# Kernel tuning notes

Measured on AMD Instinct MI355X. Metric: run time of the kernel, lower is better.

Reference implementation:

```python
import jax, jax.numpy as jnp
import numpy as np

N_NODES = 100000
N_EDGES = 1600000
IN_DIM, HID_DIM, LAT_DIM = 128, 64, 32


def glorot(key, fan_in, fan_out):
    lim = np.sqrt(6.0 / (fan_in + fan_out)).astype(np.float32)
    return jax.random.uniform(key, (fan_in, fan_out), jnp.float32, -lim, lim)


def setup_inputs() -> dict:
    key = jax.random.key(0)
    ks = jax.random.split(key, 10)
    x = jax.random.normal(ks[0], (N_NODES, IN_DIM), jnp.float32)
    edge_index = jax.random.randint(ks[1], (2, N_EDGES), 0, N_NODES, jnp.int64)
    return {
        "x": x,
        "edge_index": edge_index,
        "W1": glorot(ks[2], IN_DIM, HID_DIM), "b1": jnp.zeros((HID_DIM,), jnp.float32),
        "W2": glorot(ks[3], HID_DIM, LAT_DIM), "b2": jnp.zeros((LAT_DIM,), jnp.float32),
        "W3": glorot(ks[4], LAT_DIM, HID_DIM), "b3": jnp.zeros((HID_DIM,), jnp.float32),
        "W4": glorot(ks[5], HID_DIM, IN_DIM), "b4": jnp.zeros((IN_DIM,), jnp.float32),
    }


def gcn_conv(x, W, b, src, dst, norm_edge, norm_self):
    # x' = D^{-1/2} (A + I) D^{-1/2} x W + b  (PyG GCNConv, add_self_loops=True)
    h = x @ W                                   # [N, out]
    msg = h[src] * norm_edge[:, None]           # [E, out] gather + scale
    agg = jax.ops.segment_sum(msg, dst, num_segments=x.shape[0])  # scatter-add
    agg = agg + h * norm_self[:, None]          # self-loop contribution
    return agg + b


def reference(x, edge_index, W1, b1, W2, b2, W3, b3, W4, b4):
    src, dst = edge_index[0], edge_index[1]
    n = x.shape[0]
    # degree includes self-loop (+1); symmetric normalization
    deg = jax.ops.segment_sum(jnp.ones_like(dst, dtype=x.dtype), dst, num_segments=n) + 1.0
    dinv = jax.lax.rsqrt(deg)
    norm_edge = dinv[src] * dinv[dst]           # [E]
    norm_self = dinv * dinv                     # [N]

    # encode (dropout is identity in eval mode)
    h = jax.nn.relu(gcn_conv(x, W1, b1, src, dst, norm_edge, norm_self))
    z = gcn_conv(h, W2, b2, src, dst, norm_edge, norm_self)
    # decode
    h = jax.nn.relu(gcn_conv(z, W3, b3, src, dst, norm_edge, norm_self))
    x_rec = gcn_conv(h, W4, b4, src, dst, norm_edge, norm_self)
    return (x_rec, z)
```

## Files before the change

kernel.cpp:

```cpp
#include <hip/hip_runtime.h>
#include <hip/hip_bf16.h>

constexpr int N_NODES = 100000;
constexpr int N_EDGES = 1600000;
constexpr int SCAN_B  = 1024;
constexpr int SCAN_G  = (N_NODES + SCAN_B) / SCAN_B;
constexpr int FCH     = 8192;
constexpr int NCH     = (N_EDGES + FCH - 1) / FCH;
constexpr int SLICE_N = N_NODES / 8;
constexpr int PADC    = 48;

constexpr size_t OFF_FLAG = 0;
constexpr size_t OFF_DEG  = 4    * 1024;
constexpr size_t OFF_DINV = 408  * 1024;
constexpr size_t OFF_OFFS = 812  * 1024;
constexpr size_t OFF_CURS = 1216 * 1024;
constexpr size_t OFF_BSUM = 1620 * 1024;
constexpr size_t OFF_WC   = 1624 * 1024;
constexpr size_t OFF_CSR  = 1712 * 1024;
constexpr size_t OFF_A    = 8192 * 1024;
constexpr size_t OFF_B    = 21504ul * 1024;

constexpr size_t OFF_PAD  = 1792ul  * 1024;
constexpr size_t OFF_A2   = 20544ul * 1024;
constexpr size_t OFF_B2   = 33044ul * 1024;
constexpr size_t NEED_PAD = OFF_B2 + (size_t)N_NODES * 64 * 2;
static_assert(OFF_PAD >= OFF_WC + 20768 * 4, "pad must not clobber Wc");
static_assert(OFF_A2 >= OFF_PAD + (size_t)N_NODES * PADC * 4, "A2 overlaps pad");
static_assert(OFF_B2 >= OFF_A2 + (size_t)N_NODES * 64 * 2, "B2 overlaps A2");

constexpr int BUK_SH  = 9;
constexpr int BUK_N   = 512;
constexpr int NBUK    = (N_NODES + BUK_N - 1) / BUK_N;
constexpr int BUKCAP  = 10240;
constexpr int P1_CH   = 4096;
constexpr int P1_BLK  = (N_EDGES + P1_CH - 1) / P1_CH;
static_assert((size_t)NBUK * BUKCAP * 8 <= (size_t)N_NODES * 64 * 2 * 2, "ebuf fits A2+B2");
static_assert(NBUK * 4 <= 4096, "bucket cursors fit BSUM region");
static_assert((BUK_N * PADC * 4) % 64 == 0, "pad rows line-aligned per bucket");

constexpr int WC_W1 = 0, WC_W2 = 8192, WC_W3 = 10240, WC_W4 = 12288;
constexpr int WC_B1 = 20480, WC_B2 = 20544, WC_B3 = 20576, WC_B4 = 20640;
constexpr int WC_TOT = 20768;

__device__ __forceinline__ float bf2f(unsigned short b) {
    union { unsigned u; float f; } c; c.u = ((unsigned)b) << 16; return c.f;
}

__device__ __forceinline__ short f2bf(float f) {
    union { float f; unsigned u; } c; c.f = f;
    return (short)((c.u + 0x7FFFu + ((c.u >> 16) & 1u)) >> 16);
}

__device__ __forceinline__ int ntload(const int* p) {
    return __builtin_nontemporal_load(p);
}

__global__ void detect_kernel(const unsigned* __restrict__ w1raw,
                              const unsigned* __restrict__ eiraw,
                              int* __restrict__ flags) {
    const int t = threadIdx.x;
    int f32 = 0, i32 = 0;
    for (int i = t; i < 1024; i += 256) {
        unsigned lo = w1raw[i] & 0xFFFFu;
        if ((lo & 0x7F80u) >= 0x3F00u) f32 = 1;
    }
    for (int i = t; i < 4096; i += 256)
        if ((i & 1) && eiraw[i] != 0u) i32 = 1;
    if (f32) atomicOr(&flags[0], 1);
    if (i32) atomicOr(&flags[1], 1);
}

__device__ __forceinline__ unsigned edge_src(const int* ei, int i64, int e) {
    return (unsigned)(i64 ? ntload(&ei[2 * (size_t)e]) : ntload(&ei[e]));
}
__device__ __forceinline__ unsigned edge_dst(const int* ei, int i64, int e) {
    return (unsigned)(i64 ? ntload(&ei[2 * (size_t)N_EDGES + 2 * (size_t)e])
                          : ntload(&ei[(size_t)N_EDGES + e]));
}

__global__ void convw_kernel(const void* W1, const void* b1, const void* W2, const void* b2,
                             const void* W3, const void* b3, const void* W4, const void* b4,
                             const int* __restrict__ flags, float* __restrict__ Wc) {
    int i = blockIdx.x * blockDim.x + threadIdx.x;
    if (i >= WC_TOT) return;
    const void* src; int off;
    if      (i < WC_W2) { src = W1; off = i; }
    else if (i < WC_W3) { src = W2; off = i - WC_W2; }
    else if (i < WC_W4) { src = W3; off = i - WC_W3; }
    else if (i < WC_B1) { src = W4; off = i - WC_W4; }
    else if (i < WC_B2) { src = b1; off = i - WC_B1; }
    else if (i < WC_B3) { src = b2; off = i - WC_B2; }
    else if (i < WC_B4) { src = b3; off = i - WC_B3; }
    else                { src = b4; off = i - WC_B4; }
    Wc[i] = flags[0] ? ((const float*)src)[off]
                     : __bfloat162float(((const __hip_bfloat16*)src)[off]);
}

__global__ __launch_bounds__(256) void bsort1_kernel(
        const int* __restrict__ ei, const int* __restrict__ flags,
        int* __restrict__ gcur, int2* __restrict__ ebuf) {
    __shared__ int hist[NBUK], base[NBUK], cur[NBUK];
    const int i64 = (flags[1] == 0);
    for (int i = threadIdx.x; i < NBUK; i += 256) { hist[i] = 0; cur[i] = 0; }
    __syncthreads();
    const int e0 = blockIdx.x * P1_CH;
    const int e1 = min(e0 + P1_CH, N_EDGES);
    for (int e = e0 + threadIdx.x; e < e1; e += 256) {
        const unsigned d = edge_dst(ei, i64, e);
        const unsigned s = edge_src(ei, i64, e);
        if (d < (unsigned)N_NODES && s < (unsigned)N_NODES)
            atomicAdd(&hist[d >> BUK_SH], 1);
    }
    __syncthreads();
    for (int b = threadIdx.x; b < NBUK; b += 256)
        base[b] = hist[b] ? atomicAdd(&gcur[b], hist[b]) : 0;
    __syncthreads();
    for (int e = e0 + threadIdx.x; e < e1; e += 256) {
        const unsigned d = edge_dst(ei, i64, e);
        const unsigned s = edge_src(ei, i64, e);
        if (d < (unsigned)N_NODES && s < (unsigned)N_NODES) {
            const int b = (int)(d >> BUK_SH);
            const int p = base[b] + atomicAdd(&cur[b], 1);
            if (p < BUKCAP) ebuf[(size_t)b * BUKCAP + p] = make_int2((int)s, (int)d);
        }
    }
}

__global__ __launch_bounds__(1024) void bsort2_kernel(
        const int* __restrict__ gcur, const int2* __restrict__ ebuf,
        int* __restrict__ cnt, int* __restrict__ pad, float* __restrict__ dinv) {
    __shared__ int lc[BUK_N];
    const int b  = blockIdx.x;
    const int n0 = b * BUK_N;
    const int nn = min(BUK_N, N_NODES - n0);
    if (threadIdx.x < BUK_N) lc[threadIdx.x] = 0;
    __syncthreads();
    const int ne = min(gcur[b], BUKCAP);
    for (int i = threadIdx.x; i < ne; i += 1024) {
        const int2 p = ebuf[(size_t)b * BUKCAP + i];
        const int pos = atomicAdd(&lc[p.y - n0], 1);
        if (pos < PADC) pad[(size_t)p.y * PADC + pos] = p.x;
    }
    __syncthreads();
    for (int t = threadIdx.x; t < nn; t += 1024) {
        const int c = lc[t];
        cnt[n0 + t]  = c;
        dinv[n0 + t] = rsqrtf((float)c + 1.0f);
    }
}

__global__ void deg_kernel(const int* __restrict__ ei, const int* __restrict__ flags,
                           int* __restrict__ deg) {
    const int slice = blockIdx.x & 7;
    const int chunk = blockIdx.x >> 3;
    const int i64 = (flags[1] == 0);
    const unsigned lo = (unsigned)(slice * SLICE_N);
    const int e0 = chunk * FCH;
    const int e1 = min(e0 + FCH, N_EDGES);
    for (int e = e0 + threadIdx.x; e < e1; e += 256) {
        unsigned d = edge_dst(ei, i64, e);
        if (d - lo < (unsigned)SLICE_N && d < (unsigned)N_NODES) atomicAdd(&deg[d], 1);
    }
}

__global__ void dinv_kernel(const int* __restrict__ deg, float* __restrict__ dinv) {
    int n = blockIdx.x * blockDim.x + threadIdx.x;
    if (n < N_NODES) dinv[n] = rsqrtf((float)deg[n] + 1.0f);
}

__global__ __launch_bounds__(1024) void scan1_kernel(const int* __restrict__ deg,
                                                     int* __restrict__ bsum) {
    const int i = blockIdx.x * SCAN_B + threadIdx.x;
    const int lane = threadIdx.x & 63, wid = threadIdx.x >> 6;
    int v = (i < N_NODES) ? deg[i] : 0;
    for (int o = 32; o > 0; o >>= 1) v += __shfl_down(v, o, 64);
    __shared__ int ws[16];
    if (lane == 0) ws[wid] = v;
    __syncthreads();
    if (wid == 0) {
        int t = (lane < 16) ? ws[lane] : 0;
        for (int o = 8; o > 0; o >>= 1) t += __shfl_down(t, o, 64);
        if (lane == 0) bsum[blockIdx.x] = t;
    }
}

__global__ void scan2_kernel(const int* __restrict__ bsum, int* __restrict__ boff) {
    const int t = threadIdx.x;
    __shared__ int tmp[128];
    int v = (t < SCAN_G) ? bsum[t] : 0;
    tmp[t] = v;
    __syncthreads();
    for (int o = 1; o < 128; o <<= 1) {
        int a = (t >= o) ? tmp[t - o] : 0;
        __syncthreads();
        tmp[t] += a;
        __syncthreads();
    }
    boff[t] = tmp[t] - v;
}

__global__ __launch_bounds__(1024) void scan3_kernel(const int* __restrict__ deg,
                                                     const int* __restrict__ boff,
                                                     int* __restrict__ offs,
                                                     int* __restrict__ curs) {
    const int i = blockIdx.x * SCAN_B + threadIdx.x;
    const int lane = threadIdx.x & 63, wid = threadIdx.x >> 6;
    int v = (i < N_NODES) ? deg[i] : 0;
    int incl = v;
    for (int o = 1; o < 64; o <<= 1) {
        int t = __shfl_up(incl, (unsigned)o, 64);
        if (lane >= o) incl += t;
    }
    __shared__ int wsum[16], woff[16];
    if (lane == 63) wsum[wid] = incl;
    __syncthreads();
    if (wid == 0 && lane < 16) {
        int u = wsum[lane];
        int uin = u;
        for (int o = 1; o < 16; o <<= 1) {
            int t = __shfl_up(uin, (unsigned)o, 64);
            if (lane >= o) uin += t;
        }
        woff[lane] = uin - u;
    }
    __syncthreads();
    const int excl = incl - v + woff[wid] + boff[blockIdx.x];
    if (i <= N_NODES) {
        offs[i] = excl;
        if (i < N_NODES) curs[i] = excl;
    }
}

__global__ void fill_kernel(const int* __restrict__ ei, const int* __restrict__ flags,
                            int* __restrict__ curs, int* __restrict__ csr) {
    const int slice = blockIdx.x & 7;
    const int chunk = blockIdx.x >> 3;
    const int i64 = (flags[1] == 0);
    const unsigned lo = (unsigned)(slice * SLICE_N);
    const int e0 = chunk * FCH;
    const int e1 = min(e0 + FCH, N_EDGES);
    for (int e = e0 + threadIdx.x; e < e1; e += 256) {
        unsigned d = edge_dst(ei, i64, e);
        if (d - lo < (unsigned)SLICE_N && d < (unsigned)N_NODES) {
            unsigned s = edge_src(ei, i64, e);
            if (s < (unsigned)N_NODES) {
                int pos = atomicAdd(&curs[d], 1);
                if ((unsigned)pos < (unsigned)N_EDGES) csr[pos] = (int)s;
            }
        }
    }
}

typedef __attribute__((ext_vector_type(8))) short bf16x8;
typedef __attribute__((ext_vector_type(4))) float f32x4;

constexpr int NTILES    = N_NODES / 16;
constexpr int GEMM_GRID = 512;
static_assert(N_NODES % 16 == 0, "tile grid requires multiple of 16");

template <int IN, int OUT, bool DYNIN, bool RELU, bool BIAS, bool SCALE, bool HASWS, bool HASG>
__global__ __launch_bounds__(256) void gemm_mfma(
        const void* __restrict__ in, int inLD, const int* __restrict__ flags,
        const float* __restrict__ Wc, int WLD, const float* __restrict__ bias,
        const float* __restrict__ dinv,
        __hip_bfloat16* __restrict__ wsout,
        void* __restrict__ gout, int gLD) {
    constexpr int KS = IN / 32;
    constexpr int NT = OUT / 16;
    static_assert(IN % 32 == 0 && OUT % 16 == 0, "shape");
    const int lane = threadIdx.x & 63;
    const int wid  = threadIdx.x >> 6;
    const int m = lane & 15;
    const int g = lane >> 4;
    const int f32f = flags[0];

    bf16x8 bfrag[NT][KS];
#pragma unroll
    for (int t = 0; t < NT; ++t) {
#pragma unroll
        for (int ks = 0; ks < KS; ++ks) {
            const float* wp = Wc + (size_t)(ks * 32 + g * 8) * WLD + t * 16 + m;
            bf16x8 b;
#pragma unroll
            for (int j = 0; j < 8; ++j) b[j] = f2bf(wp[(size_t)j * WLD]);
            bfrag[t][ks] = b;
        }
    }
    float bb[NT];
    if (BIAS) {
#pragma unroll
        for (int t = 0; t < NT; ++t) bb[t] = bias[t * 16 + m];
    }

    for (int tile = blockIdx.x * 4 + wid; tile < NTILES; tile += GEMM_GRID * 4) {
        f32x4 acc[NT];
#pragma unroll
        for (int t = 0; t < NT; ++t) {
            const float b0 = BIAS ? bb[t] : 0.0f;
            acc[t] = (f32x4){b0, b0, b0, b0};
        }
        const size_t arow = (size_t)tile * 16 + m;
#pragma unroll
        for (int ks = 0; ks < KS; ++ks) {
            bf16x8 af;
            if (DYNIN && f32f) {
                const float* xp = (const float*)in + arow * inLD + ks * 32 + g * 8;
                const float4 v0 = *(const float4*)xp;
                const float4 v1 = *(const float4*)(xp + 4);
                af[0] = f2bf(v0.x); af[1] = f2bf(v0.y);
                af[2] = f2bf(v0.z); af[3] = f2bf(v0.w);
                af[4] = f2bf(v1.x); af[5] = f2bf(v1.y);
                af[6] = f2bf(v1.z); af[7] = f2bf(v1.w);
            } else {
                af = *(const bf16x8*)((const __hip_bfloat16*)in + arow * inLD + ks * 32 + g * 8);
            }
#pragma unroll
            for (int t = 0; t < NT; ++t)
                acc[t] = __builtin_amdgcn_mfma_f32_16x16x32_bf16(af, bfrag[t][ks], acc[t], 0, 0, 0);
        }
        const int rbase = tile * 16 + g * 4;
        float di[4];
        if (SCALE) {
#pragma unroll
            for (int r = 0; r < 4; ++r) di[r] = dinv[rbase + r];
        }
#pragma unroll
        for (int t = 0; t < NT; ++t) {
            const int col = t * 16 + m;
#pragma unroll
            for (int r = 0; r < 4; ++r) {
                float v = acc[t][r];
                if (RELU) v = fmaxf(v, 0.0f);
                if (SCALE) v *= di[r];
                const size_t row = (size_t)(rbase + r);
                if (HASWS) wsout[row * OUT + col] = __float2bfloat16(v);
                if (HASG) {
                    const size_t gi = row * gLD + col;
                    if (f32f) ((float*)gout)[gi] = v;
                    else      ((__hip_bfloat16*)gout)[gi] = __float2bfloat16(v);
                }
            }
        }
    }
}

template <int D, int SUBW, bool RELU, bool PADDED>
__global__ __launch_bounds__(256) void agg_kernel(
        const int* __restrict__ base, const int* __restrict__ adj,
        const float* __restrict__ dinv,
        const __hip_bfloat16* __restrict__ h,
        const float* __restrict__ bias,
        __hip_bfloat16* __restrict__ wsout,
        __hip_bfloat16* __restrict__ wsout_sc,
        void* __restrict__ gout, size_t gbase, int gLD,
        const int* __restrict__ flags) {
    const int lane = threadIdx.x & 63;
    const int wid  = threadIdx.x >> 6;
    constexpr int SPW = 64 / SUBW;
    constexpr int SPB = 4 * SPW;
    const int n = blockIdx.x * SPB + wid * SPW + (SUBW == 64 ? 0 : (lane >> 5));
    if (n >= N_NODES) return;
    const int sl = lane & (SUBW - 1);
    const int col = sl;
    float acc = __bfloat162float(h[(size_t)n * D + col]);
    int o0, o1;
    if (PADDED) {
        o0 = n * PADC;
        o1 = o0 + min(base[n], PADC);
    } else {
        o0 = base[n]; o1 = base[n + 1];
    }
    for (int bse = o0; bse < o1; bse += SUBW) {
        const int idx = bse + sl;
        const int sid = (idx < o1) ? adj[idx] : 0;
        const int cnt = min(SUBW, o1 - bse);
        int k = 0;
        for (; k + 8 <= cnt; k += 8) {
            int s[8];
#pragma unroll
            for (int u = 0; u < 8; ++u) s[u] = __shfl(sid, k + u, SUBW);
            float v[8];
#pragma unroll
            for (int u = 0; u < 8; ++u) v[u] = __bfloat162float(h[(size_t)s[u] * D + col]);
            acc += ((v[0] + v[1]) + (v[2] + v[3])) + ((v[4] + v[5]) + (v[6] + v[7]));
        }
        for (; k < cnt; ++k) {
            const int s = __shfl(sid, k, SUBW);
            acc += __bfloat162float(h[(size_t)s * D + col]);
        }
    }
    const float di = dinv[n];
    float v = acc * di;
    if (bias) v += bias[col];
    if (RELU) v = fmaxf(v, 0.0f);
    if (wsout)    wsout[(size_t)n * D + col]    = __float2bfloat16(v);
    if (wsout_sc) wsout_sc[(size_t)n * D + col] = __float2bfloat16(v * di);
    if (gout) {
        const size_t gi = gbase + (size_t)n * gLD + col;
        if (flags[0]) ((float*)gout)[gi] = v;
        else          ((__hip_bfloat16*)gout)[gi] = __float2bfloat16(v);
    }
}

template <bool P>
static inline void run_layers(const void* x, const int* flags, float* Wc, float* dinv,
                              const int* base, const int* adj,
                              __hip_bfloat16* A, __hip_bfloat16* B,
                              void* d_out, hipStream_t stream) {
    gemm_mfma<128, 64, true, false, false, true, true, false><<<GEMM_GRID, 256, 0, stream>>>(
        x, 128, flags, Wc + WC_W1, 64, nullptr, dinv, A, nullptr, 0);
    agg_kernel<64, 64, true, P><<<(N_NODES + 3) / 4, 256, 0, stream>>>(
        base, adj, dinv, A, Wc + WC_B1, B, nullptr, nullptr, 0, 0, flags);

    gemm_mfma<64, 32, false, false, false, true, true, false><<<GEMM_GRID, 256, 0, stream>>>(
        B, 64, flags, Wc + WC_W2, 32, nullptr, dinv, A, nullptr, 0);
    agg_kernel<32, 32, false, P><<<(N_NODES + 7) / 8, 256, 0, stream>>>(
        base, adj, dinv, A, Wc + WC_B2, nullptr, B,
        d_out, (size_t)N_NODES * 128, 32, flags);

    agg_kernel<32, 32, false, P><<<(N_NODES + 7) / 8, 256, 0, stream>>>(
        base, adj, dinv, B, nullptr, A, nullptr, nullptr, 0, 0, flags);
    gemm_mfma<32, 64, false, true, true, true, true, false><<<GEMM_GRID, 256, 0, stream>>>(
        A, 32, flags, Wc + WC_W3, 64, Wc + WC_B3, dinv, B, nullptr, 0);

    agg_kernel<64, 64, false, P><<<(N_NODES + 3) / 4, 256, 0, stream>>>(
        base, adj, dinv, B, nullptr, A, nullptr, nullptr, 0, 0, flags);
    gemm_mfma<64, 128, false, false, true, false, false, true><<<GEMM_GRID, 256, 0, stream>>>(
        A, 64, flags, Wc + WC_W4, 128, Wc + WC_B4, dinv, nullptr, d_out, 128);
}

extern "C" void kernel_launch(void* const* d_in, const int* in_sizes, int n_in,
                              void* d_out, int out_size, void* d_ws, size_t ws_size,
                              hipStream_t stream) {
    const void* x  = d_in[0];
    const int* ei  = (const int*)d_in[1];
    const void* W1 = d_in[2]; const void* b1 = d_in[3];
    const void* W2 = d_in[4]; const void* b2 = d_in[5];
    const void* W3 = d_in[6]; const void* b3 = d_in[7];
    const void* W4 = d_in[8]; const void* b4 = d_in[9];

    char* ws = (char*)d_ws;
    int*   flags = (int*)(ws + OFF_FLAG);
    int*   cnt   = (int*)(ws + OFF_DEG);
    float* dinv  = (float*)(ws + OFF_DINV);
    float* Wc    = (float*)(ws + OFF_WC);

    hipMemsetAsync(flags, 0, 2 * sizeof(int), stream);
    hipMemsetAsync(cnt, 0, (size_t)N_NODES * sizeof(int), stream);
    detect_kernel<<<1, 256, 0, stream>>>((const unsigned*)W1, (const unsigned*)ei, flags);
    convw_kernel<<<(WC_TOT + 255) / 256, 256, 0, stream>>>(W1, b1, W2, b2, W3, b3, W4, b4,
                                                           flags, Wc);

    if (ws_size >= NEED_PAD) {
        int*  pad  = (int*)(ws + OFF_PAD);
        int*  gcur = (int*)(ws + OFF_BSUM);
        int2* ebuf = (int2*)(ws + OFF_A2);
        __hip_bfloat16* A = (__hip_bfloat16*)(ws + OFF_A2);
        __hip_bfloat16* B = (__hip_bfloat16*)(ws + OFF_B2);
        hipMemsetAsync(gcur, 0, NBUK * sizeof(int), stream);
        bsort1_kernel<<<P1_BLK, 256, 0, stream>>>(ei, flags, gcur, ebuf);
        bsort2_kernel<<<NBUK, 1024, 0, stream>>>(gcur, ebuf, cnt, pad, dinv);
        run_layers<true>(x, flags, Wc, dinv, cnt, pad, A, B, d_out, stream);
    } else {
        int*   offs  = (int*)(ws + OFF_OFFS);
        int*   curs  = (int*)(ws + OFF_CURS);
        int*   bsum  = (int*)(ws + OFF_BSUM);
        int*   boff  = bsum + 128;
        int*   csr   = (int*)(ws + OFF_CSR);
        __hip_bfloat16* A = (__hip_bfloat16*)(ws + OFF_A);
        __hip_bfloat16* B = (__hip_bfloat16*)(ws + OFF_B);
        deg_kernel<<<8 * NCH, 256, 0, stream>>>(ei, flags, cnt);
        dinv_kernel<<<(N_NODES + 255) / 256, 256, 0, stream>>>(cnt, dinv);
        scan1_kernel<<<SCAN_G, SCAN_B, 0, stream>>>(cnt, bsum);
        scan2_kernel<<<1, 128, 0, stream>>>(bsum, boff);
        scan3_kernel<<<SCAN_G, SCAN_B, 0, stream>>>(cnt, boff, offs, curs);
        fill_kernel<<<8 * NCH, 256, 0, stream>>>(ei, flags, curs, csr);
        run_layers<false>(x, flags, Wc, dinv, offs, csr, A, B, d_out, stream);
    }
}
```

Measured before the change: 392.6 us.

## Fuse aggregation with small GEMMs and pack bucket-sort edge records

```diff
diff --git a/kernel.cpp b/kernel.cpp
--- a/kernel.cpp
+++ b/kernel.cpp
@@ -35,9 +35,9 @@
 constexpr int BUKCAP  = 10240;
 constexpr int P1_CH   = 4096;
 constexpr int P1_BLK  = (N_EDGES + P1_CH - 1) / P1_CH;
-static_assert((size_t)NBUK * BUKCAP * 8 <= (size_t)N_NODES * 64 * 2 * 2, "ebuf fits A2+B2");
+static_assert((size_t)NBUK * BUKCAP * 4 <= (size_t)N_NODES * 64 * 2, "ebuf fits A2");
 static_assert(NBUK * 4 <= 4096, "bucket cursors fit BSUM region");
-static_assert((BUK_N * PADC * 4) % 64 == 0, "pad rows line-aligned per bucket");
+static_assert(NBUK < 255, "bucket id fits uchar with 0xFF sentinel");
 
 constexpr int WC_W1 = 0, WC_W2 = 8192, WC_W3 = 10240, WC_W4 = 12288;
 constexpr int WC_B1 = 20480, WC_B2 = 20544, WC_B3 = 20576, WC_B4 = 20640;
@@ -99,36 +99,42 @@
 
 __global__ __launch_bounds__(256) void bsort1_kernel(
         const int* __restrict__ ei, const int* __restrict__ flags,
-        int* __restrict__ gcur, int2* __restrict__ ebuf) {
-    __shared__ int hist[NBUK], base[NBUK], cur[NBUK];
+        int* __restrict__ gcur, int* __restrict__ ebuf) {
+    __shared__ int hist[NBUK], rbase[NBUK], cur[NBUK];
+    __shared__ int pk[P1_CH];
+    __shared__ unsigned char bk[P1_CH];
     const int i64 = (flags[1] == 0);
     for (int i = threadIdx.x; i < NBUK; i += 256) { hist[i] = 0; cur[i] = 0; }
     __syncthreads();
     const int e0 = blockIdx.x * P1_CH;
-    const int e1 = min(e0 + P1_CH, N_EDGES);
-    for (int e = e0 + threadIdx.x; e < e1; e += 256) {
-        const unsigned d = edge_dst(ei, i64, e);
-        const unsigned s = edge_src(ei, i64, e);
-        if (d < (unsigned)N_NODES && s < (unsigned)N_NODES)
-            atomicAdd(&hist[d >> BUK_SH], 1);
-    }
-    __syncthreads();
-    for (int b = threadIdx.x; b < NBUK; b += 256)
-        base[b] = hist[b] ? atomicAdd(&gcur[b], hist[b]) : 0;
-    __syncthreads();
-    for (int e = e0 + threadIdx.x; e < e1; e += 256) {
-        const unsigned d = edge_dst(ei, i64, e);
-        const unsigned s = edge_src(ei, i64, e);
+    const int ne = min(P1_CH, N_EDGES - e0);
+    for (int i = threadIdx.x; i < ne; i += 256) {
+        const unsigned d = edge_dst(ei, i64, e0 + i);
+        const unsigned s = edge_src(ei, i64, e0 + i);
         if (d < (unsigned)N_NODES && s < (unsigned)N_NODES) {
             const int b = (int)(d >> BUK_SH);
-            const int p = base[b] + atomicAdd(&cur[b], 1);
-            if (p < BUKCAP) ebuf[(size_t)b * BUKCAP + p] = make_int2((int)s, (int)d);
+            atomicAdd(&hist[b], 1);
+            bk[i] = (unsigned char)b;
+            pk[i] = (int)(((d & (BUK_N - 1)) << 17) | s);
+        } else {
+            bk[i] = 0xFF;
+        }
+    }
+    __syncthreads();
+    for (int b = threadIdx.x; b < NBUK; b += 256)
+        rbase[b] = hist[b] ? atomicAdd(&gcur[b], hist[b]) : 0;
+    __syncthreads();
+    for (int i = threadIdx.x; i < ne; i += 256) {
+        const int b = bk[i];
+        if (b != 0xFF) {
+            const int p = rbase[b] + atomicAdd(&cur[b], 1);
+            if (p < BUKCAP) ebuf[(size_t)b * BUKCAP + p] = pk[i];
         }
     }
 }
 
 __global__ __launch_bounds__(1024) void bsort2_kernel(
-        const int* __restrict__ gcur, const int2* __restrict__ ebuf,
+        const int* __restrict__ gcur, const int* __restrict__ ebuf,
         int* __restrict__ cnt, int* __restrict__ pad, float* __restrict__ dinv) {
     __shared__ int lc[BUK_N];
     const int b  = blockIdx.x;
@@ -138,9 +144,11 @@
     __syncthreads();
     const int ne = min(gcur[b], BUKCAP);
     for (int i = threadIdx.x; i < ne; i += 1024) {
-        const int2 p = ebuf[(size_t)b * BUKCAP + i];
-        const int pos = atomicAdd(&lc[p.y - n0], 1);
-        if (pos < PADC) pad[(size_t)p.y * PADC + pos] = p.x;
+        const int v = ebuf[(size_t)b * BUKCAP + i];
+        const int dloc = v >> 17;
+        const int s = v & 0x1FFFF;
+        const int pos = atomicAdd(&lc[dloc], 1);
+        if (pos < PADC) pad[(size_t)(n0 + dloc) * PADC + pos] = s;
     }
     __syncthreads();
     for (int t = threadIdx.x; t < nn; t += 1024) {
@@ -403,6 +411,104 @@
     }
 }
 
+__global__ __launch_bounds__(256) void aggmm1_kernel(
+        const int* __restrict__ cnt, const int* __restrict__ pad,
+        const float* __restrict__ dinv,
+        const __hip_bfloat16* __restrict__ h,
+        const float* __restrict__ W2,
+        const float* __restrict__ b1,
+        __hip_bfloat16* __restrict__ out32) {
+    __shared__ float Ws[64 * 32];
+    __shared__ float Xs[4][64];
+    const int tid = threadIdx.x;
+    for (int i = tid; i < 64 * 32; i += 256) Ws[i] = W2[i];
+    __syncthreads();
+    const int lane = tid & 63, wid = tid >> 6;
+    const int n = blockIdx.x * 4 + wid;
+    float acc = __bfloat162float(h[(size_t)n * 64 + lane]);
+    const int o0 = n * PADC;
+    const int o1 = o0 + min(cnt[n], PADC);
+    for (int bse = o0; bse < o1; bse += 64) {
+        const int idx = bse + lane;
+        const int sid = (idx < o1) ? pad[idx] : 0;
+        const int cn = min(64, o1 - bse);
+        int k = 0;
+        for (; k + 8 <= cn; k += 8) {
+            int s[8];
+#pragma unroll
+            for (int u = 0; u < 8; ++u) s[u] = __shfl(sid, k + u, 64);
+            float v[8];
+#pragma unroll
+            for (int u = 0; u < 8; ++u) v[u] = __bfloat162float(h[(size_t)s[u] * 64 + lane]);
+            acc += ((v[0] + v[1]) + (v[2] + v[3])) + ((v[4] + v[5]) + (v[6] + v[7]));
+        }
+        for (; k < cn; ++k) {
+            const int s = __shfl(sid, k, 64);
+            acc += __bfloat162float(h[(size_t)s * 64 + lane]);
+        }
+    }
+    const float di = dinv[n];
+    Xs[wid][lane] = fmaxf(acc * di + b1[lane], 0.0f);
+    const int j = lane & 31;
+    float o = 0.0f;
+#pragma unroll 8
+    for (int k = 0; k < 64; ++k) o = fmaf(Xs[wid][k], Ws[k * 32 + j], o);
+    if (lane < 32) out32[(size_t)n * 32 + j] = __float2bfloat16(o * di);
+}
+
+__global__ __launch_bounds__(256) void aggmm3_kernel(
+        const int* __restrict__ cnt, const int* __restrict__ pad,
+        const float* __restrict__ dinv,
+        const __hip_bfloat16* __restrict__ h,
+        const float* __restrict__ W3,
+        const float* __restrict__ b3,
+        __hip_bfloat16* __restrict__ out64) {
+    __shared__ float Ws[32 * 64];
+    __shared__ float Xs[8][32];
+    const int tid = threadIdx.x;
+    for (int i = tid; i < 32 * 64; i += 256) Ws[i] = W3[i];
+    __syncthreads();
+    const int lane = tid & 63, wid = tid >> 6;
+    const int sub = lane >> 5, sl = lane & 31;
+    const int sw = wid * 2 + sub;
+    const int n = blockIdx.x * 8 + sw;
+    float acc = __bfloat162float(h[(size_t)n * 32 + sl]);
+    const int o0 = n * PADC;
+    const int o1 = o0 + min(cnt[n], PADC);
+    for (int bse = o0; bse < o1; bse += 32) {
+        const int idx = bse + sl;
+        const int sid = (idx < o1) ? pad[idx] : 0;
+        const int cn = min(32, o1 - bse);
+        int k = 0;
+        for (; k + 8 <= cn; k += 8) {
+            int s[8];
+#pragma unroll
+            for (int u = 0; u < 8; ++u) s[u] = __shfl(sid, k + u, 32);
+            float v[8];
+#pragma unroll
+            for (int u = 0; u < 8; ++u) v[u] = __bfloat162float(h[(size_t)s[u] * 32 + sl]);
+            acc += ((v[0] + v[1]) + (v[2] + v[3])) + ((v[4] + v[5]) + (v[6] + v[7]));
+        }
+        for (; k < cn; ++k) {
+            const int s = __shfl(sid, k, 32);
+            acc += __bfloat162float(h[(size_t)s * 32 + sl]);
+        }
+    }
+    const float di = dinv[n];
+    Xs[sw][sl] = acc * di;
+    float p0 = 0.0f, p1 = 0.0f;
+#pragma unroll 8
+    for (int k = 0; k < 32; ++k) {
+        const float a = Xs[sw][k];
+        p0 = fmaf(a, Ws[k * 64 + sl], p0);
+        p1 = fmaf(a, Ws[k * 64 + sl + 32], p1);
+    }
+    p0 = fmaxf(p0 + b3[sl], 0.0f) * di;
+    p1 = fmaxf(p1 + b3[sl + 32], 0.0f) * di;
+    out64[(size_t)n * 64 + sl]      = __float2bfloat16(p0);
+    out64[(size_t)n * 64 + sl + 32] = __float2bfloat16(p1);
+}
+
 template <bool P>
 static inline void run_layers(const void* x, const int* flags, float* Wc, float* dinv,
                               const int* base, const int* adj,
@@ -412,18 +518,15 @@
         x, 128, flags, Wc + WC_W1, 64, nullptr, dinv, A, nullptr, 0);
     agg_kernel<64, 64, true, P><<<(N_NODES + 3) / 4, 256, 0, stream>>>(
         base, adj, dinv, A, Wc + WC_B1, B, nullptr, nullptr, 0, 0, flags);
-
     gemm_mfma<64, 32, false, false, false, true, true, false><<<GEMM_GRID, 256, 0, stream>>>(
         B, 64, flags, Wc + WC_W2, 32, nullptr, dinv, A, nullptr, 0);
     agg_kernel<32, 32, false, P><<<(N_NODES + 7) / 8, 256, 0, stream>>>(
         base, adj, dinv, A, Wc + WC_B2, nullptr, B,
         d_out, (size_t)N_NODES * 128, 32, flags);
-
     agg_kernel<32, 32, false, P><<<(N_NODES + 7) / 8, 256, 0, stream>>>(
         base, adj, dinv, B, nullptr, A, nullptr, nullptr, 0, 0, flags);
     gemm_mfma<32, 64, false, true, true, true, true, false><<<GEMM_GRID, 256, 0, stream>>>(
         A, 32, flags, Wc + WC_W3, 64, Wc + WC_B3, dinv, B, nullptr, 0);
-
     agg_kernel<64, 64, false, P><<<(N_NODES + 3) / 4, 256, 0, stream>>>(
         base, adj, dinv, B, nullptr, A, nullptr, nullptr, 0, 0, flags);
     gemm_mfma<64, 128, false, false, true, false, false, true><<<GEMM_GRID, 256, 0, stream>>>(
@@ -455,13 +558,28 @@
     if (ws_size >= NEED_PAD) {
         int*  pad  = (int*)(ws + OFF_PAD);
         int*  gcur = (int*)(ws + OFF_BSUM);
-        int2* ebuf = (int2*)(ws + OFF_A2);
-        __hip_bfloat16* A = (__hip_bfloat16*)(ws + OFF_A2);
-        __hip_bfloat16* B = (__hip_bfloat16*)(ws + OFF_B2);
+        int*  ebuf = (int*)(ws + OFF_A2);
+        __hip_bfloat16* A   = (__hip_bfloat16*)(ws + OFF_A2);
+        __hip_bfloat16* C32 = (__hip_bfloat16*)(ws + OFF_B2);
+        __hip_bfloat16* D32 = C32 + (size_t)N_NODES * 32;
+        __hip_bfloat16* B   = (__hip_bfloat16*)(ws + OFF_B2);
         hipMemsetAsync(gcur, 0, NBUK * sizeof(int), stream);
         bsort1_kernel<<<P1_BLK, 256, 0, stream>>>(ei, flags, gcur, ebuf);
         bsort2_kernel<<<NBUK, 1024, 0, stream>>>(gcur, ebuf, cnt, pad, dinv);
-        run_layers<true>(x, flags, Wc, dinv, cnt, pad, A, B, d_out, stream);
+
+        gemm_mfma<128, 64, true, false, false, true, true, false><<<GEMM_GRID, 256, 0, stream>>>(
+            x, 128, flags, Wc + WC_W1, 64, nullptr, dinv, A, nullptr, 0);
+        aggmm1_kernel<<<N_NODES / 4, 256, 0, stream>>>(
+            cnt, pad, dinv, A, Wc + WC_W2, Wc + WC_B1, C32);
+        agg_kernel<32, 32, false, true><<<(N_NODES + 7) / 8, 256, 0, stream>>>(
+            cnt, pad, dinv, C32, Wc + WC_B2, nullptr, D32,
+            d_out, (size_t)N_NODES * 128, 32, flags);
+        aggmm3_kernel<<<N_NODES / 8, 256, 0, stream>>>(
+            cnt, pad, dinv, D32, Wc + WC_W3, Wc + WC_B3, A);
+        agg_kernel<64, 64, false, true><<<(N_NODES + 3) / 4, 256, 0, stream>>>(
+            cnt, pad, dinv, A, nullptr, B, nullptr, nullptr, 0, 0, flags);
+        gemm_mfma<64, 128, false, false, true, false, false, true><<<GEMM_GRID, 256, 0, stream>>>(
+            B, 64, flags, Wc + WC_W4, 128, Wc + WC_B4, dinv, nullptr, d_out, 128);
     } else {
         int*   offs  = (int*)(ws + OFF_OFFS);
         int*   curs  = (int*)(ws + OFF_CURS);
```

Result: slower. 405.2 us (+3.2%).

## Vectorize GCN aggregation with packed bucket-sort edges and 4-wide bf16 gathers

Applied to the files above, without the earlier changes.

```diff
diff --git a/kernel.cpp b/kernel.cpp
--- a/kernel.cpp
+++ b/kernel.cpp
@@ -35,9 +35,9 @@
 constexpr int BUKCAP  = 10240;
 constexpr int P1_CH   = 4096;
 constexpr int P1_BLK  = (N_EDGES + P1_CH - 1) / P1_CH;
-static_assert((size_t)NBUK * BUKCAP * 8 <= (size_t)N_NODES * 64 * 2 * 2, "ebuf fits A2+B2");
+static_assert((size_t)NBUK * BUKCAP * 4 <= (size_t)N_NODES * 64 * 2, "ebuf fits A2");
 static_assert(NBUK * 4 <= 4096, "bucket cursors fit BSUM region");
-static_assert((BUK_N * PADC * 4) % 64 == 0, "pad rows line-aligned per bucket");
+static_assert(NBUK < 255, "bucket id fits uchar with 0xFF sentinel");
 
 constexpr int WC_W1 = 0, WC_W2 = 8192, WC_W3 = 10240, WC_W4 = 12288;
 constexpr int WC_B1 = 20480, WC_B2 = 20544, WC_B3 = 20576, WC_B4 = 20640;
@@ -99,36 +99,42 @@
 
 __global__ __launch_bounds__(256) void bsort1_kernel(
         const int* __restrict__ ei, const int* __restrict__ flags,
-        int* __restrict__ gcur, int2* __restrict__ ebuf) {
-    __shared__ int hist[NBUK], base[NBUK], cur[NBUK];
+        int* __restrict__ gcur, int* __restrict__ ebuf) {
+    __shared__ int hist[NBUK], rbase[NBUK], cur[NBUK];
+    __shared__ int pk[P1_CH];
+    __shared__ unsigned char bk[P1_CH];
     const int i64 = (flags[1] == 0);
     for (int i = threadIdx.x; i < NBUK; i += 256) { hist[i] = 0; cur[i] = 0; }
     __syncthreads();
     const int e0 = blockIdx.x * P1_CH;
-    const int e1 = min(e0 + P1_CH, N_EDGES);
-    for (int e = e0 + threadIdx.x; e < e1; e += 256) {
-        const unsigned d = edge_dst(ei, i64, e);
-        const unsigned s = edge_src(ei, i64, e);
-        if (d < (unsigned)N_NODES && s < (unsigned)N_NODES)
-            atomicAdd(&hist[d >> BUK_SH], 1);
-    }
-    __syncthreads();
-    for (int b = threadIdx.x; b < NBUK; b += 256)
-        base[b] = hist[b] ? atomicAdd(&gcur[b], hist[b]) : 0;
-    __syncthreads();
-    for (int e = e0 + threadIdx.x; e < e1; e += 256) {
-        const unsigned d = edge_dst(ei, i64, e);
-        const unsigned s = edge_src(ei, i64, e);
+    const int ne = min(P1_CH, N_EDGES - e0);
+    for (int i = threadIdx.x; i < ne; i += 256) {
+        const unsigned d = edge_dst(ei, i64, e0 + i);
+        const unsigned s = edge_src(ei, i64, e0 + i);
         if (d < (unsigned)N_NODES && s < (unsigned)N_NODES) {
             const int b = (int)(d >> BUK_SH);
-            const int p = base[b] + atomicAdd(&cur[b], 1);
-            if (p < BUKCAP) ebuf[(size_t)b * BUKCAP + p] = make_int2((int)s, (int)d);
+            atomicAdd(&hist[b], 1);
+            bk[i] = (unsigned char)b;
+            pk[i] = (int)(((d & (BUK_N - 1)) << 17) | s);
+        } else {
+            bk[i] = 0xFF;
+        }
+    }
+    __syncthreads();
+    for (int b = threadIdx.x; b < NBUK; b += 256)
+        rbase[b] = hist[b] ? atomicAdd(&gcur[b], hist[b]) : 0;
+    __syncthreads();
+    for (int i = threadIdx.x; i < ne; i += 256) {
+        const int b = bk[i];
+        if (b != 0xFF) {
+            const int p = rbase[b] + atomicAdd(&cur[b], 1);
+            if (p < BUKCAP) ebuf[(size_t)b * BUKCAP + p] = pk[i];
         }
     }
 }
 
 __global__ __launch_bounds__(1024) void bsort2_kernel(
-        const int* __restrict__ gcur, const int2* __restrict__ ebuf,
+        const int* __restrict__ gcur, const int* __restrict__ ebuf,
         int* __restrict__ cnt, int* __restrict__ pad, float* __restrict__ dinv) {
     __shared__ int lc[BUK_N];
     const int b  = blockIdx.x;
@@ -138,9 +144,11 @@
     __syncthreads();
     const int ne = min(gcur[b], BUKCAP);
     for (int i = threadIdx.x; i < ne; i += 1024) {
-        const int2 p = ebuf[(size_t)b * BUKCAP + i];
-        const int pos = atomicAdd(&lc[p.y - n0], 1);
-        if (pos < PADC) pad[(size_t)p.y * PADC + pos] = p.x;
+        const int v = ebuf[(size_t)b * BUKCAP + i];
+        const int dloc = v >> 17;
+        const int s = v & 0x1FFFF;
+        const int pos = atomicAdd(&lc[dloc], 1);
+        if (pos < PADC) pad[(size_t)(n0 + dloc) * PADC + pos] = s;
     }
     __syncthreads();
     for (int t = threadIdx.x; t < nn; t += 1024) {
@@ -403,6 +411,92 @@
     }
 }
 
+template <int D, bool RELU>
+__global__ __launch_bounds__(256) void aggv_kernel(
+        const int* __restrict__ cnt, const int* __restrict__ pad,
+        const float* __restrict__ dinv,
+        const __hip_bfloat16* __restrict__ h,
+        const float* __restrict__ bias,
+        __hip_bfloat16* __restrict__ wsout,
+        __hip_bfloat16* __restrict__ wsout_sc,
+        void* __restrict__ gout, size_t gbase, int gLD,
+        const int* __restrict__ flags) {
+    constexpr int SW  = D / 4;
+    constexpr int NPW = 64 / SW;
+    constexpr int NPB = 4 * NPW;
+    static_assert(N_NODES % NPB == 0, "exact grid");
+    const int lane = threadIdx.x & 63;
+    const int wid  = threadIdx.x >> 6;
+    const int sub  = lane / SW;
+    const int sl   = lane % SW;
+    const int n = blockIdx.x * NPB + wid * NPW + sub;
+    const int col = sl * 4;
+    float a0, a1, a2, a3;
+    {
+        const ushort4 u = *(const ushort4*)&h[(size_t)n * D + col];
+        a0 = bf2f(u.x); a1 = bf2f(u.y); a2 = bf2f(u.z); a3 = bf2f(u.w);
+    }
+    const int o0 = n * PADC;
+    const int o1 = o0 + min(cnt[n], PADC);
+    for (int bse = o0; bse < o1; bse += SW) {
+        const int idx = bse + sl;
+        const int sid = (idx < o1) ? pad[idx] : 0;
+        const int cn = min(SW, o1 - bse);
+        int k = 0;
+        for (; k + 8 <= cn; k += 8) {
+            int s[8];
+#pragma unroll
+            for (int u = 0; u < 8; ++u) s[u] = __shfl(sid, k + u, SW);
+            ushort4 v[8];
+#pragma unroll
+            for (int u = 0; u < 8; ++u) v[u] = *(const ushort4*)&h[(size_t)s[u] * D + col];
+            a0 += ((bf2f(v[0].x) + bf2f(v[1].x)) + (bf2f(v[2].x) + bf2f(v[3].x))) +
+                  ((bf2f(v[4].x) + bf2f(v[5].x)) + (bf2f(v[6].x) + bf2f(v[7].x)));
+            a1 += ((bf2f(v[0].y) + bf2f(v[1].y)) + (bf2f(v[2].y) + bf2f(v[3].y))) +
+                  ((bf2f(v[4].y) + bf2f(v[5].y)) + (bf2f(v[6].y) + bf2f(v[7].y)));
+            a2 += ((bf2f(v[0].z) + bf2f(v[1].z)) + (bf2f(v[2].z) + bf2f(v[3].z))) +
+                  ((bf2f(v[4].z) + bf2f(v[5].z)) + (bf2f(v[6].z) + bf2f(v[7].z)));
+            a3 += ((bf2f(v[0].w) + bf2f(v[1].w)) + (bf2f(v[2].w) + bf2f(v[3].w))) +
+                  ((bf2f(v[4].w) + bf2f(v[5].w)) + (bf2f(v[6].w) + bf2f(v[7].w)));
+        }
+        for (; k < cn; ++k) {
+            const int s = __shfl(sid, k, SW);
+            const ushort4 u = *(const ushort4*)&h[(size_t)s * D + col];
+            a0 += bf2f(u.x); a1 += bf2f(u.y); a2 += bf2f(u.z); a3 += bf2f(u.w);
+        }
+    }
+    const float di = dinv[n];
+    float v0 = a0 * di, v1 = a1 * di, v2 = a2 * di, v3 = a3 * di;
+    if (bias) {
+        v0 += bias[col]; v1 += bias[col + 1]; v2 += bias[col + 2]; v3 += bias[col + 3];
+    }
+    if (RELU) {
+        v0 = fmaxf(v0, 0.0f); v1 = fmaxf(v1, 0.0f);
+        v2 = fmaxf(v2, 0.0f); v3 = fmaxf(v3, 0.0f);
+    }
+    if (wsout) {
+        ushort4 o; o.x = (unsigned short)f2bf(v0); o.y = (unsigned short)f2bf(v1);
+        o.z = (unsigned short)f2bf(v2); o.w = (unsigned short)f2bf(v3);
+        *(ushort4*)&wsout[(size_t)n * D + col] = o;
+    }
+    if (wsout_sc) {
+        ushort4 o; o.x = (unsigned short)f2bf(v0 * di); o.y = (unsigned short)f2bf(v1 * di);
+        o.z = (unsigned short)f2bf(v2 * di); o.w = (unsigned short)f2bf(v3 * di);
+        *(ushort4*)&wsout_sc[(size_t)n * D + col] = o;
+    }
+    if (gout) {
+        const size_t gi = gbase + (size_t)n * gLD + col;
+        if (flags[0]) {
+            float4 o = {v0, v1, v2, v3};
+            *(float4*)&((float*)gout)[gi] = o;
+        } else {
+            ushort4 o; o.x = (unsigned short)f2bf(v0); o.y = (unsigned short)f2bf(v1);
+            o.z = (unsigned short)f2bf(v2); o.w = (unsigned short)f2bf(v3);
+            *(ushort4*)&((__hip_bfloat16*)gout)[gi] = o;
+        }
+    }
+}
+
 template <bool P>
 static inline void run_layers(const void* x, const int* flags, float* Wc, float* dinv,
                               const int* base, const int* adj,
@@ -412,18 +506,15 @@
         x, 128, flags, Wc + WC_W1, 64, nullptr, dinv, A, nullptr, 0);
     agg_kernel<64, 64, true, P><<<(N_NODES + 3) / 4, 256, 0, stream>>>(
         base, adj, dinv, A, Wc + WC_B1, B, nullptr, nullptr, 0, 0, flags);
-
     gemm_mfma<64, 32, false, false, false, true, true, false><<<GEMM_GRID, 256, 0, stream>>>(
         B, 64, flags, Wc + WC_W2, 32, nullptr, dinv, A, nullptr, 0);
     agg_kernel<32, 32, false, P><<<(N_NODES + 7) / 8, 256, 0, stream>>>(
         base, adj, dinv, A, Wc + WC_B2, nullptr, B,
         d_out, (size_t)N_NODES * 128, 32, flags);
-
     agg_kernel<32, 32, false, P><<<(N_NODES + 7) / 8, 256, 0, stream>>>(
         base, adj, dinv, B, nullptr, A, nullptr, nullptr, 0, 0, flags);
     gemm_mfma<32, 64, false, true, true, true, true, false><<<GEMM_GRID, 256, 0, stream>>>(
         A, 32, flags, Wc + WC_W3, 64, Wc + WC_B3, dinv, B, nullptr, 0);
-
     agg_kernel<64, 64, false, P><<<(N_NODES + 3) / 4, 256, 0, stream>>>(
         base, adj, dinv, B, nullptr, A, nullptr, nullptr, 0, 0, flags);
     gemm_mfma<64, 128, false, false, true, false, false, true><<<GEMM_GRID, 256, 0, stream>>>(
@@ -455,13 +546,30 @@
     if (ws_size >= NEED_PAD) {
         int*  pad  = (int*)(ws + OFF_PAD);
         int*  gcur = (int*)(ws + OFF_BSUM);
-        int2* ebuf = (int2*)(ws + OFF_A2);
+        int*  ebuf = (int*)(ws + OFF_A2);
         __hip_bfloat16* A = (__hip_bfloat16*)(ws + OFF_A2);
         __hip_bfloat16* B = (__hip_bfloat16*)(ws + OFF_B2);
         hipMemsetAsync(gcur, 0, NBUK * sizeof(int), stream);
         bsort1_kernel<<<P1_BLK, 256, 0, stream>>>(ei, flags, gcur, ebuf);
         bsort2_kernel<<<NBUK, 1024, 0, stream>>>(gcur, ebuf, cnt, pad, dinv);
-        run_layers<true>(x, flags, Wc, dinv, cnt, pad, A, B, d_out, stream);
+
+        gemm_mfma<128, 64, true, false, false, true, true, false><<<GEMM_GRID, 256, 0, stream>>>(
+            x, 128, flags, Wc + WC_W1, 64, nullptr, dinv, A, nullptr, 0);
+        aggv_kernel<64, true><<<N_NODES / 16, 256, 0, stream>>>(
+            cnt, pad, dinv, A, Wc + WC_B1, B, nullptr, nullptr, 0, 0, flags);
+        gemm_mfma<64, 32, false, false, false, true, true, false><<<GEMM_GRID, 256, 0, stream>>>(
+            B, 64, flags, Wc + WC_W2, 32, nullptr, dinv, A, nullptr, 0);
+        aggv_kernel<32, false><<<N_NODES / 32, 256, 0, stream>>>(
+            cnt, pad, dinv, A, Wc + WC_B2, nullptr, B,
+            d_out, (size_t)N_NODES * 128, 32, flags);
+        aggv_kernel<32, false><<<N_NODES / 32, 256, 0, stream>>>(
+            cnt, pad, dinv, B, nullptr, A, nullptr, nullptr, 0, 0, flags);
+        gemm_mfma<32, 64, false, true, true, true, true, false><<<GEMM_GRID, 256, 0, stream>>>(
+            A, 32, flags, Wc + WC_W3, 64, Wc + WC_B3, dinv, B, nullptr, 0);
+        aggv_kernel<64, false><<<N_NODES / 16, 256, 0, stream>>>(
+            cnt, pad, dinv, B, nullptr, A, nullptr, nullptr, 0, 0, flags);
+        gemm_mfma<64, 128, false, false, true, false, false, true><<<GEMM_GRID, 256, 0, stream>>>(
+            A, 64, flags, Wc + WC_W4, 128, Wc + WC_B4, dinv, nullptr, d_out, 128);
     } else {
         int*   offs  = (int*)(ws + OFF_OFFS);
         int*   curs  = (int*)(ws + OFF_CURS);
```

After: 339.9 us. -13.4%, faster.
